# Kernel optimization log

Measured on AMD Instinct MI355X. Metric: run time of the kernel, lower is better.

The kernel has to match this reference:

```python
import jax, jax.numpy as jnp
import numpy as np

N = 50000
E = 800000
HID = 128
EIN = 2 * HID + 1  # h[row] ++ h[col] ++ edge_attr
NC = 3             # n_coords
DIM = 3            # spatial dim
NORM_FACTOR = 100.0
LN_EPS = 1e-5


def layernorm(x, g, b):
    m = jnp.mean(x, axis=-1, keepdims=True)
    v = jnp.mean(jnp.square(x - m), axis=-1, keepdims=True)
    return (x - m) * jax.lax.rsqrt(v + LN_EPS) * g + b


def setup_inputs() -> dict:
    key = jax.random.key(0)
    ks = jax.random.split(key, 12)
    h = jax.random.normal(ks[0], (N, HID), dtype=jnp.float32)
    coord = jax.random.normal(ks[1], (N, NC, DIM), dtype=jnp.float32)
    coord_diff = jax.random.normal(ks[2], (E, NC, DIM), dtype=jnp.float32)
    edge_attr = jax.random.normal(ks[3], (E, 1), dtype=jnp.float32)
    edge_mask = jnp.ones((E, 1), dtype=jnp.float32)
    node_mask = jnp.ones((N, 1, 1), dtype=jnp.float32)
    row = jax.random.randint(ks[4], (E,), 0, N, dtype=jnp.int32)
    col = jax.random.randint(ks[5], (E,), 0, N, dtype=jnp.int32)
    # MLP params (stored [in, out])
    def xavier(k, fi, fo, gain=1.0):
        lim = gain * np.sqrt(6.0 / (fi + fo))
        return jax.random.uniform(k, (fi, fo), dtype=jnp.float32, minval=-lim, maxval=lim)
    W1 = xavier(ks[6], EIN, HID)
    b1 = jnp.zeros((HID,), jnp.float32)
    g1 = jnp.ones((HID,), jnp.float32)
    be1 = jnp.zeros((HID,), jnp.float32)
    W2 = xavier(ks[7], HID, HID)
    b2 = jnp.zeros((HID,), jnp.float32)
    g2 = jnp.ones((HID,), jnp.float32)
    be2 = jnp.zeros((HID,), jnp.float32)
    W3 = xavier(ks[8], HID, NC * NC, gain=0.01)  # final layer, no bias
    return dict(h=h, coord=coord, coord_diff=coord_diff, edge_attr=edge_attr,
                edge_mask=edge_mask, node_mask=node_mask, row=row, col=col,
                W1=W1, b1=b1, g1=g1, be1=be1, W2=W2, b2=b2, g2=g2, be2=be2, W3=W3)


def reference(h, coord, coord_diff, edge_attr, edge_mask, node_mask, row, col,
              W1, b1, g1, be1, W2, b2, g2, be2, W3):
    # gather node feats into edge features: [E, 2*HID + 1]
    x = jnp.concatenate([h[row], h[col], edge_attr], axis=1)
    x = jax.nn.silu(layernorm(x @ W1 + b1, g1, be1))
    x = jax.nn.silu(layernorm(x @ W2 + b2, g2, be2))
    phi = (x @ W3).reshape(-1, NC, NC)               # [E, NC, NC]
    trans = jnp.einsum('ejk,ejl->elk', coord_diff, phi)  # [E, NC, DIM]
    trans = trans * edge_mask[:, None]               # [E,1,1] broadcast
    agg = jax.ops.segment_sum(trans, row, num_segments=coord.shape[0]) / NORM_FACTOR
    return (coord + agg) * node_mask
```

## Files before the change

kernel.cpp:

```cpp
#include <hip/hip_runtime.h>
#include <hip/hip_bf16.h>

#define NN 50000
#define EE 800000

typedef __attribute__((ext_vector_type(8))) short short8;
typedef __attribute__((ext_vector_type(4))) short short4v;
typedef __attribute__((ext_vector_type(4))) float f32x4;

__device__ __forceinline__ float bf2f(ushort u) {
  union { unsigned u; float f; } v; v.u = ((unsigned)u) << 16; return v.f;
}
__device__ __forceinline__ ushort f2bf(float f) {
  union { float f; unsigned u; } v; v.f = f;
  unsigned r = v.u + 0x7FFFu + ((v.u >> 16) & 1u);
  return (ushort)(r >> 16);
}
__device__ __forceinline__ float silu(float v) {
  return v * __builtin_amdgcn_rcpf(1.f + __expf(-v));
}

__global__ void prep_kernel(const float* __restrict__ W1, const float* __restrict__ W2,
                            const float* __restrict__ W3,
                            ushort* __restrict__ W1at, ushort* __restrict__ W1bt,
                            ushort* __restrict__ W2t, ushort* __restrict__ W3t,
                            float* __restrict__ agg) {
  int b = blockIdx.x, tid = threadIdx.x;
  if (b < 200) {
    int i = b * 256 + tid;
    if (i < 16384) {
      int n = i >> 7, k = i & 127;
      W1at[i] = f2bf(W1[k*128 + n]);
    } else if (i < 32768) {
      int j = i - 16384, n = j >> 7, k = j & 127;
      W1bt[j] = f2bf(W1[(k + 128)*128 + n]);
    } else if (i < 49152) {
      int j = i - 32768, n = j >> 7, k = j & 127;
      W2t[j] = f2bf(W2[k*128 + n]);
    } else if (i < 51200) {
      int j = i - 49152, n = j >> 7, k = j & 127;
      W3t[j] = (n < 9) ? f2bf(W3[k*9 + n]) : (ushort)0;
    }
  } else {
    int i = (b - 200) * 256 + tid;
    if (i < NN*9) agg[i] = 0.f;
  }
}

template<bool PQF32>
__global__ __launch_bounds__(256, 4)
void node_kernel(const float* __restrict__ h,
                 const ushort* __restrict__ W1at, const ushort* __restrict__ W1bt,
                 const float* __restrict__ b1,
                 void* __restrict__ Pv, void* __restrict__ Qv) {
  __shared__ __align__(16) ushort smH[64*128];
  const int tid = threadIdx.x;
  const int lane = tid & 63;
  const int w   = tid >> 6;
  const int l15 = lane & 15;
  const int lh  = lane >> 4;
  const int wm  = w >> 1;
  const int wn  = w & 1;
  const int n0  = blockIdx.x * 64;

  {
    int e = tid >> 2, p = tid & 3;
    int nn = n0 + e; if (nn >= NN) nn = NN - 1;
    const float* s = h + (size_t)nn*128 + p*32;
    #pragma unroll
    for (int c = 0; c < 4; ++c) {
      float4 a = *(const float4*)(s + c*8);
      float4 bq = *(const float4*)(s + c*8 + 4);
      short8 v;
      v[0]=f2bf(a.x); v[1]=f2bf(a.y); v[2]=f2bf(a.z); v[3]=f2bf(a.w);
      v[4]=f2bf(bq.x); v[5]=f2bf(bq.y); v[6]=f2bf(bq.z); v[7]=f2bf(bq.w);
      int bo = (e*256 + p*64 + c*16) ^ ((e & 7) << 4);
      *(short8*)((char*)smH + bo) = v;
    }
  }
  __syncthreads();

  const ushort* W = wm ? W1bt : W1at;
  f32x4 acc[4][2] = {};
  #pragma unroll
  for (int k0 = 0; k0 < 4; ++k0) {
    short8 a[4], b[2];
    #pragma unroll
    for (int mf = 0; mf < 4; ++mf)
      a[mf] = *(const short8*)(W + (size_t)(mf*16 + l15)*128 + k0*32 + lh*8);
    #pragma unroll
    for (int nf = 0; nf < 2; ++nf) {
      int e = wn*32 + nf*16 + l15;
      int bo = (e*256 + k0*64 + lh*16) ^ ((e & 7) << 4);
      b[nf] = *(const short8*)((char*)smH + bo);
    }
    #pragma unroll
    for (int mf = 0; mf < 4; ++mf)
      #pragma unroll
      for (int nf = 0; nf < 2; ++nf)
        acc[mf][nf] = __builtin_amdgcn_mfma_f32_16x16x32_bf16(a[mf], b[nf], acc[mf][nf], 0, 0, 0);
  }

  #pragma unroll
  for (int mf = 0; mf < 4; ++mf) {
    float4 bq = *(const float4*)(b1 + mf*16 + lh*4);
    #pragma unroll
    for (int nf = 0; nf < 2; ++nf) {
      int node = n0 + wn*32 + nf*16 + l15;
      if (node < NN) {
        f32x4 r = acc[mf][nf];
        if (wm == 0) { r[0]+=bq.x; r[1]+=bq.y; r[2]+=bq.z; r[3]+=bq.w; }
        if (PQF32) {
          float* dst = (float*)(wm ? Qv : Pv) + (size_t)node*128 + mf*16 + lh*4;
          *(f32x4*)dst = r;
        } else {
          ushort* dst = (ushort*)(wm ? Qv : Pv) + (size_t)node*128 + mf*16 + lh*4;
          short4v o; o[0]=f2bf(r[0]); o[1]=f2bf(r[1]); o[2]=f2bf(r[2]); o[3]=f2bf(r[3]);
          *(short4v*)dst = o;
        }
      }
    }
  }
}

template<bool PQF32>
__global__ __launch_bounds__(256, 6)
void edge_kernel(const void* __restrict__ Pv, const void* __restrict__ Qv,
                 const float* __restrict__ w1last,
                 const float* __restrict__ g1, const float* __restrict__ be1,
                 const ushort* __restrict__ W2t, const ushort* __restrict__ W3t,
                 const float* __restrict__ b2, const float* __restrict__ g2, const float* __restrict__ be2,
                 const float* __restrict__ edge_attr, const float* __restrict__ edge_mask,
                 const float* __restrict__ coord_diff,
                 const int* __restrict__ row, const int* __restrict__ col,
                 float* __restrict__ agg) {
  __shared__ __align__(16) char smem[25344];
  ushort* smX   = (ushort*)smem;
  float*  smPhi = (float*)(smem + 16384);
  float*  smCd  = (float*)(smem + 21504);
  float2* smRed = (float2*)(smem + 23808);
  float*  smEM  = (float*)(smem + 24832);
  int*    smRow = (int*)  (smem + 25088);

  const int tid  = threadIdx.x;
  const int lane = tid & 63;
  const int w    = tid >> 6;
  const int l15  = lane & 15;
  const int lh   = lane >> 4;
  const int wm   = w >> 1;
  const int wn   = w & 1;
  const int e0   = blockIdx.x * 64;
  const int nb   = wm*64 + lh*4;

  {
    int e = tid >> 2, p = tid & 3;
    int re = row[e0 + e], ce = col[e0 + e];
    float ea = edge_attr[e0 + e];
    if (p == 0) { smEM[e] = edge_mask[e0+e]; smRow[e] = re; }

    float v[32]; float s = 0.f, q = 0.f;
    if (PQF32) {
      const float* Pp = (const float*)Pv + (size_t)re*128 + p*32;
      const float* Qp = (const float*)Qv + (size_t)ce*128 + p*32;
      #pragma unroll
      for (int c = 0; c < 8; ++c) {
        float4 a = *(const float4*)(Pp + c*4);
        float4 bq = *(const float4*)(Qp + c*4);
        float4 wq = *(const float4*)(w1last + p*32 + c*4);
        #pragma unroll
        for (int j = 0; j < 4; ++j) {
          float t = ((const float*)&a)[j] + ((const float*)&bq)[j] + ea * ((const float*)&wq)[j];
          v[c*4 + j] = t; s += t; q += t*t;
        }
      }
    } else {
      const ushort* Pp = (const ushort*)Pv + (size_t)re*128 + p*32;
      const ushort* Qp = (const ushort*)Qv + (size_t)ce*128 + p*32;
      #pragma unroll
      for (int c = 0; c < 4; ++c) {
        short8 a = *(const short8*)(Pp + c*8);
        short8 bq = *(const short8*)(Qp + c*8);
        float4 wq0 = *(const float4*)(w1last + p*32 + c*8);
        float4 wq1 = *(const float4*)(w1last + p*32 + c*8 + 4);
        #pragma unroll
        for (int j = 0; j < 8; ++j) {
          float wv = (j < 4) ? ((const float*)&wq0)[j] : ((const float*)&wq1)[j-4];
          float t = bf2f((ushort)a[j]) + bf2f((ushort)bq[j]) + ea * wv;
          v[c*8 + j] = t; s += t; q += t*t;
        }
      }
    }
    s += __shfl_xor(s, 1, 64); s += __shfl_xor(s, 2, 64);
    q += __shfl_xor(q, 1, 64); q += __shfl_xor(q, 2, 64);
    float m  = s * (1.f/128.f);
    float rs = rsqrtf(q * (1.f/128.f) - m*m + 1e-5f);
    #pragma unroll
    for (int c = 0; c < 4; ++c) {
      float4 gq0 = *(const float4*)(g1 + p*32 + c*8);
      float4 gq1 = *(const float4*)(g1 + p*32 + c*8 + 4);
      float4 bq0 = *(const float4*)(be1 + p*32 + c*8);
      float4 bq1 = *(const float4*)(be1 + p*32 + c*8 + 4);
      short8 o;
      #pragma unroll
      for (int j = 0; j < 8; ++j) {
        float gv = (j < 4) ? ((const float*)&gq0)[j] : ((const float*)&gq1)[j-4];
        float bv = (j < 4) ? ((const float*)&bq0)[j] : ((const float*)&bq1)[j-4];
        float val = (v[c*8+j] - m) * rs * gv + bv;
        o[j] = f2bf(silu(val));
      }
      int bo = (e*256 + p*64 + c*16) ^ ((e & 7) << 4);
      *(short8*)((char*)smX + bo) = o;
    }
  }
  if (tid < 144)
    *(float4*)(smCd + tid*4) = *(const float4*)(coord_diff + (size_t)e0*9 + tid*4);
  __syncthreads();

  f32x4 acc2[4][2] = {};
  {
    const ushort* A2 = W2t + (size_t)(wm*64 + l15) * 128 + lh*8;
    #pragma unroll
    for (int k0 = 0; k0 < 4; ++k0) {
      short8 a[4], b[2];
      #pragma unroll
      for (int mf = 0; mf < 4; ++mf) a[mf] = *(const short8*)(A2 + mf*2048 + k0*32);
      #pragma unroll
      for (int nf = 0; nf < 2; ++nf) {
        int e = wn*32 + nf*16 + l15;
        int bo = (e*256 + k0*64 + lh*16) ^ ((e & 7) << 4);
        b[nf] = *(const short8*)((char*)smX + bo);
      }
      #pragma unroll
      for (int mf = 0; mf < 4; ++mf)
        #pragma unroll
        for (int nf = 0; nf < 2; ++nf)
          acc2[mf][nf] = __builtin_amdgcn_mfma_f32_16x16x32_bf16(a[mf], b[nf], acc2[mf][nf], 0, 0, 0);
    }
  }

  float s2[2] = {0.f, 0.f}, q2[2] = {0.f, 0.f};
  #pragma unroll
  for (int mf = 0; mf < 4; ++mf) {
    float4 b2q = *(const float4*)(b2 + nb + mf*16);
    #pragma unroll
    for (int nf = 0; nf < 2; ++nf)
      #pragma unroll
      for (int j = 0; j < 4; ++j) {
        float t = acc2[mf][nf][j] + ((const float*)&b2q)[j];
        acc2[mf][nf][j] = t; s2[nf] += t; q2[nf] += t*t;
      }
  }
  #pragma unroll
  for (int nf = 0; nf < 2; ++nf) {
    s2[nf] += __shfl_xor(s2[nf], 16, 64); s2[nf] += __shfl_xor(s2[nf], 32, 64);
    q2[nf] += __shfl_xor(q2[nf], 16, 64); q2[nf] += __shfl_xor(q2[nf], 32, 64);
  }
  if (lh == 0) {
    #pragma unroll
    for (int nf = 0; nf < 2; ++nf)
      smRed[((wm*2 + wn)*2 + nf)*16 + l15] = make_float2(s2[nf], q2[nf]);
  }
  __syncthreads();

  {
    float m[2], rs[2];
    #pragma unroll
    for (int nf = 0; nf < 2; ++nf) {
      float2 po = smRed[(((wm^1)*2 + wn)*2 + nf)*16 + l15];
      float S = s2[nf] + po.x, Q = q2[nf] + po.y;
      m[nf] = S * (1.f/128.f);
      rs[nf] = rsqrtf(Q * (1.f/128.f) - m[nf]*m[nf] + 1e-5f);
    }
    #pragma unroll
    for (int mf = 0; mf < 4; ++mf) {
      float4 gq  = *(const float4*)(g2 + nb + mf*16);
      float4 beq = *(const float4*)(be2 + nb + mf*16);
      #pragma unroll
      for (int nf = 0; nf < 2; ++nf) {
        int e = wn*32 + nf*16 + l15;
        short4v o;
        #pragma unroll
        for (int j = 0; j < 4; ++j) {
          float val = (acc2[mf][nf][j] - m[nf]) * rs[nf] * ((const float*)&gq)[j] + ((const float*)&beq)[j];
          o[j] = f2bf(silu(val));
        }
        int bo = (e*256 + (nb + mf*16)*2) ^ ((e & 7) << 4);
        *(short4v*)((char*)smX + bo) = o;
      }
    }
  }
  __syncthreads();

  {
    f32x4 acc3 = {};
    const ushort* A3 = W3t + (size_t)l15 * 128 + lh*8;
    int e = w*16 + l15;
    #pragma unroll
    for (int k0 = 0; k0 < 4; ++k0) {
      short8 a = *(const short8*)(A3 + k0*32);
      int bo = (e*256 + k0*64 + lh*16) ^ ((e & 7) << 4);
      short8 b = *(const short8*)((char*)smX + bo);
      acc3 = __builtin_amdgcn_mfma_f32_16x16x32_bf16(a, b, acc3, 0, 0, 0);
    }
    *(float4*)(smPhi + e*20 + lh*4) = *(float4*)&acc3;
  }
  __syncthreads();

  {
    int e = tid >> 2, qd = tid & 3;
    int re = smRow[e];
    float em = smEM[e];
    const float* cd = smCd + e*9;
    const float* ph = smPhi + e*20;
    for (int idx = qd; idx < 9; idx += 4) {
      int l2 = idx / 3, k = idx - l2*3;
      float t = cd[k]*ph[l2] + cd[3+k]*ph[3+l2] + cd[6+k]*ph[6+l2];
      unsafeAtomicAdd(&agg[(size_t)re*9 + idx], t * em);
    }
  }
}

__global__ void finalize_kernel(const float* __restrict__ coord, const float* __restrict__ node_mask,
                                const float* __restrict__ agg, float* __restrict__ out) {
  int i = blockIdx.x * 256 + threadIdx.x;
  if (i < NN*9) {
    int n = i / 9;
    out[i] = (coord[i] + agg[i] * 0.01f) * node_mask[n];
  }
}

extern "C" void kernel_launch(void* const* d_in, const int* in_sizes, int n_in,
                              void* d_out, int out_size, void* d_ws, size_t ws_size,
                              hipStream_t stream) {
  const float* h          = (const float*)d_in[0];
  const float* coord      = (const float*)d_in[1];
  const float* coord_diff = (const float*)d_in[2];
  const float* edge_attr  = (const float*)d_in[3];
  const float* edge_mask  = (const float*)d_in[4];
  const float* node_mask  = (const float*)d_in[5];
  const int*   rowi       = (const int*)d_in[6];
  const int*   coli       = (const int*)d_in[7];
  const float* W1  = (const float*)d_in[8];
  const float* b1  = (const float*)d_in[9];
  const float* g1  = (const float*)d_in[10];
  const float* be1 = (const float*)d_in[11];
  const float* W2  = (const float*)d_in[12];
  const float* b2  = (const float*)d_in[13];
  const float* g2  = (const float*)d_in[14];
  const float* be2 = (const float*)d_in[15];
  const float* W3  = (const float*)d_in[16];
  const float* w1last = W1 + 256*128;

  char* ws = (char*)d_ws;
  const size_t needF32 = 53102400;
  const int nodeBlocks = (NN + 63) / 64;
  const int aggBlocks  = (NN*9 + 255) / 256;

  if (ws_size >= needF32) {
    float*  P    = (float*)ws;
    float*  Q    = (float*)(ws + 25600000);
    float*  agg  = (float*)(ws + 51200000);
    ushort* W1at = (ushort*)(ws + 53000000);
    ushort* W1bt = (ushort*)(ws + 53032768);
    ushort* W2t  = (ushort*)(ws + 53065536);
    ushort* W3t  = (ushort*)(ws + 53098304);
    prep_kernel<<<200 + aggBlocks, 256, 0, stream>>>(W1, W2, W3, W1at, W1bt, W2t, W3t, agg);
    node_kernel<true><<<nodeBlocks, 256, 0, stream>>>(h, W1at, W1bt, b1, P, Q);
    edge_kernel<true><<<EE/64, 256, 0, stream>>>(P, Q, w1last, g1, be1, W2t, W3t,
        b2, g2, be2, edge_attr, edge_mask, coord_diff, rowi, coli, agg);
    finalize_kernel<<<aggBlocks, 256, 0, stream>>>(coord, node_mask, agg, (float*)d_out);
  } else {
    ushort* P    = (ushort*)ws;
    ushort* Q    = (ushort*)(ws + 12800000);
    float*  agg  = (float*)(ws + 25600000);
    ushort* W1at = (ushort*)(ws + 27400000);
    ushort* W1bt = (ushort*)(ws + 27432768);
    ushort* W2t  = (ushort*)(ws + 27465536);
    ushort* W3t  = (ushort*)(ws + 27498304);
    prep_kernel<<<200 + aggBlocks, 256, 0, stream>>>(W1, W2, W3, W1at, W1bt, W2t, W3t, agg);
    node_kernel<false><<<nodeBlocks, 256, 0, stream>>>(h, W1at, W1bt, b1, P, Q);
    edge_kernel<false><<<EE/64, 256, 0, stream>>>(P, Q, w1last, g1, be1, W2t, W3t,
        b2, g2, be2, edge_attr, edge_mask, coord_diff, rowi, coli, agg);
    finalize_kernel<<<aggBlocks, 256, 0, stream>>>(coord, node_mask, agg, (float*)d_out);
  }
}
```

Baseline: 536.3 us.

## Make edge kernel wave-local with bf16 P/Q and no block barriers

```diff
diff --git a/kernel.cpp b/kernel.cpp
--- a/kernel.cpp
+++ b/kernel.cpp
@@ -47,12 +47,11 @@
   }
 }
 
-template<bool PQF32>
 __global__ __launch_bounds__(256, 4)
 void node_kernel(const float* __restrict__ h,
                  const ushort* __restrict__ W1at, const ushort* __restrict__ W1bt,
                  const float* __restrict__ b1,
-                 void* __restrict__ Pv, void* __restrict__ Qv) {
+                 ushort* __restrict__ P, ushort* __restrict__ Q) {
   __shared__ __align__(16) ushort smH[64*128];
   const int tid = threadIdx.x;
   const int lane = tid & 63;
@@ -110,22 +109,16 @@
       if (node < NN) {
         f32x4 r = acc[mf][nf];
         if (wm == 0) { r[0]+=bq.x; r[1]+=bq.y; r[2]+=bq.z; r[3]+=bq.w; }
-        if (PQF32) {
-          float* dst = (float*)(wm ? Qv : Pv) + (size_t)node*128 + mf*16 + lh*4;
-          *(f32x4*)dst = r;
-        } else {
-          ushort* dst = (ushort*)(wm ? Qv : Pv) + (size_t)node*128 + mf*16 + lh*4;
-          short4v o; o[0]=f2bf(r[0]); o[1]=f2bf(r[1]); o[2]=f2bf(r[2]); o[3]=f2bf(r[3]);
-          *(short4v*)dst = o;
-        }
+        ushort* dst = (wm ? Q : P) + (size_t)node*128 + mf*16 + lh*4;
+        short4v o; o[0]=f2bf(r[0]); o[1]=f2bf(r[1]); o[2]=f2bf(r[2]); o[3]=f2bf(r[3]);
+        *(short4v*)dst = o;
       }
     }
   }
 }
 
-template<bool PQF32>
-__global__ __launch_bounds__(256, 6)
-void edge_kernel(const void* __restrict__ Pv, const void* __restrict__ Qv,
+__global__ __launch_bounds__(256, 4)
+void edge_kernel(const ushort* __restrict__ P, const ushort* __restrict__ Q,
                  const float* __restrict__ w1last,
                  const float* __restrict__ g1, const float* __restrict__ be1,
                  const ushort* __restrict__ W2t, const ushort* __restrict__ W3t,
@@ -134,60 +127,46 @@
                  const float* __restrict__ coord_diff,
                  const int* __restrict__ row, const int* __restrict__ col,
                  float* __restrict__ agg) {
-  __shared__ __align__(16) char smem[25344];
+  __shared__ __align__(16) char smem[23808];
   ushort* smX   = (ushort*)smem;
   float*  smPhi = (float*)(smem + 16384);
   float*  smCd  = (float*)(smem + 21504);
-  float2* smRed = (float2*)(smem + 23808);
-  float*  smEM  = (float*)(smem + 24832);
-  int*    smRow = (int*)  (smem + 25088);
 
   const int tid  = threadIdx.x;
   const int lane = tid & 63;
   const int w    = tid >> 6;
   const int l15  = lane & 15;
   const int lh   = lane >> 4;
-  const int wm   = w >> 1;
-  const int wn   = w & 1;
   const int e0   = blockIdx.x * 64;
-  const int nb   = wm*64 + lh*4;
+  const int we   = w * 16;
 
   {
     int e = tid >> 2, p = tid & 3;
-    int re = row[e0 + e], ce = col[e0 + e];
-    float ea = edge_attr[e0 + e];
-    if (p == 0) { smEM[e] = edge_mask[e0+e]; smRow[e] = re; }
+    int ge = e0 + e;
+    int re = row[ge], ce = col[ge];
+    float ea = edge_attr[ge];
+    const ushort* Pp = P + (size_t)re*128 + p*32;
+    const ushort* Qp = Q + (size_t)ce*128 + p*32;
+    short8 pa[4], qa[4];
+    #pragma unroll
+    for (int c = 0; c < 4; ++c) pa[c] = *(const short8*)(Pp + c*8);
+    #pragma unroll
+    for (int c = 0; c < 4; ++c) qa[c] = *(const short8*)(Qp + c*8);
+
+    if (lane < 36)
+      *(float4*)(smCd + we*9 + lane*4) =
+          *(const float4*)(coord_diff + (size_t)(e0 + we)*9 + lane*4);
 
     float v[32]; float s = 0.f, q = 0.f;
-    if (PQF32) {
-      const float* Pp = (const float*)Pv + (size_t)re*128 + p*32;
-      const float* Qp = (const float*)Qv + (size_t)ce*128 + p*32;
+    #pragma unroll
+    for (int c = 0; c < 4; ++c) {
+      float4 wq0 = *(const float4*)(w1last + p*32 + c*8);
+      float4 wq1 = *(const float4*)(w1last + p*32 + c*8 + 4);
       #pragma unroll
-      for (int c = 0; c < 8; ++c) {
-        float4 a = *(const float4*)(Pp + c*4);
-        float4 bq = *(const float4*)(Qp + c*4);
-        float4 wq = *(const float4*)(w1last + p*32 + c*4);
-        #pragma unroll
-        for (int j = 0; j < 4; ++j) {
-          float t = ((const float*)&a)[j] + ((const float*)&bq)[j] + ea * ((const float*)&wq)[j];
-          v[c*4 + j] = t; s += t; q += t*t;
-        }
-      }
-    } else {
-      const ushort* Pp = (const ushort*)Pv + (size_t)re*128 + p*32;
-      const ushort* Qp = (const ushort*)Qv + (size_t)ce*128 + p*32;
-      #pragma unroll
-      for (int c = 0; c < 4; ++c) {
-        short8 a = *(const short8*)(Pp + c*8);
-        short8 bq = *(const short8*)(Qp + c*8);
-        float4 wq0 = *(const float4*)(w1last + p*32 + c*8);
-        float4 wq1 = *(const float4*)(w1last + p*32 + c*8 + 4);
-        #pragma unroll
-        for (int j = 0; j < 8; ++j) {
-          float wv = (j < 4) ? ((const float*)&wq0)[j] : ((const float*)&wq1)[j-4];
-          float t = bf2f((ushort)a[j]) + bf2f((ushort)bq[j]) + ea * wv;
-          v[c*8 + j] = t; s += t; q += t*t;
-        }
+      for (int j = 0; j < 8; ++j) {
+        float wv = (j < 4) ? ((const float*)&wq0)[j] : ((const float*)&wq1)[j-4];
+        float t = bf2f((ushort)pa[c][j]) + bf2f((ushort)qa[c][j]) + ea * wv;
+        v[c*8 + j] = t; s += t; q += t*t;
       }
     }
     s += __shfl_xor(s, 1, 64); s += __shfl_xor(s, 2, 64);
@@ -212,110 +191,81 @@
       *(short8*)((char*)smX + bo) = o;
     }
   }
-  if (tid < 144)
-    *(float4*)(smCd + tid*4) = *(const float4*)(coord_diff + (size_t)e0*9 + tid*4);
-  __syncthreads();
-
-  f32x4 acc2[4][2] = {};
+  asm volatile("s_waitcnt lgkmcnt(0)" ::: "memory");
+  __builtin_amdgcn_sched_barrier(0);
+
+  const int e2 = we + l15;
+
+  f32x4 acc2[8] = {};
+  #pragma unroll
+  for (int k0 = 0; k0 < 4; ++k0) {
+    int bo = (e2*256 + k0*64 + lh*16) ^ ((e2 & 7) << 4);
+    short8 bfrag = *(const short8*)((char*)smX + bo);
+    #pragma unroll
+    for (int mf = 0; mf < 8; ++mf) {
+      short8 a = *(const short8*)(W2t + (size_t)(mf*16 + l15)*128 + k0*32 + lh*8);
+      acc2[mf] = __builtin_amdgcn_mfma_f32_16x16x32_bf16(a, bfrag, acc2[mf], 0, 0, 0);
+    }
+  }
+
+  float s2 = 0.f, q2 = 0.f;
+  #pragma unroll
+  for (int mf = 0; mf < 8; ++mf) {
+    float4 bq = *(const float4*)(b2 + mf*16 + lh*4);
+    #pragma unroll
+    for (int j = 0; j < 4; ++j) {
+      float t = acc2[mf][j] + ((const float*)&bq)[j];
+      acc2[mf][j] = t; s2 += t; q2 += t*t;
+    }
+  }
+  s2 += __shfl_xor(s2, 16, 64); s2 += __shfl_xor(s2, 32, 64);
+  q2 += __shfl_xor(q2, 16, 64); q2 += __shfl_xor(q2, 32, 64);
   {
-    const ushort* A2 = W2t + (size_t)(wm*64 + l15) * 128 + lh*8;
-    #pragma unroll
-    for (int k0 = 0; k0 < 4; ++k0) {
-      short8 a[4], b[2];
-      #pragma unroll
-      for (int mf = 0; mf < 4; ++mf) a[mf] = *(const short8*)(A2 + mf*2048 + k0*32);
-      #pragma unroll
-      for (int nf = 0; nf < 2; ++nf) {
-        int e = wn*32 + nf*16 + l15;
-        int bo = (e*256 + k0*64 + lh*16) ^ ((e & 7) << 4);
-        b[nf] = *(const short8*)((char*)smX + bo);
-      }
-      #pragma unroll
-      for (int mf = 0; mf < 4; ++mf)
-        #pragma unroll
-        for (int nf = 0; nf < 2; ++nf)
-          acc2[mf][nf] = __builtin_amdgcn_mfma_f32_16x16x32_bf16(a[mf], b[nf], acc2[mf][nf], 0, 0, 0);
-    }
-  }
-
-  float s2[2] = {0.f, 0.f}, q2[2] = {0.f, 0.f};
-  #pragma unroll
-  for (int mf = 0; mf < 4; ++mf) {
-    float4 b2q = *(const float4*)(b2 + nb + mf*16);
-    #pragma unroll
-    for (int nf = 0; nf < 2; ++nf)
+    float m  = s2 * (1.f/128.f);
+    float rs = rsqrtf(q2 * (1.f/128.f) - m*m + 1e-5f);
+    #pragma unroll
+    for (int mf = 0; mf < 8; ++mf) {
+      float4 gq  = *(const float4*)(g2 + mf*16 + lh*4);
+      float4 beq = *(const float4*)(be2 + mf*16 + lh*4);
+      short4v o;
       #pragma unroll
       for (int j = 0; j < 4; ++j) {
-        float t = acc2[mf][nf][j] + ((const float*)&b2q)[j];
-        acc2[mf][nf][j] = t; s2[nf] += t; q2[nf] += t*t;
+        float val = (acc2[mf][j] - m) * rs * ((const float*)&gq)[j] + ((const float*)&beq)[j];
+        o[j] = f2bf(silu(val));
       }
-  }
-  #pragma unroll
-  for (int nf = 0; nf < 2; ++nf) {
-    s2[nf] += __shfl_xor(s2[nf], 16, 64); s2[nf] += __shfl_xor(s2[nf], 32, 64);
-    q2[nf] += __shfl_xor(q2[nf], 16, 64); q2[nf] += __shfl_xor(q2[nf], 32, 64);
-  }
-  if (lh == 0) {
-    #pragma unroll
-    for (int nf = 0; nf < 2; ++nf)
-      smRed[((wm*2 + wn)*2 + nf)*16 + l15] = make_float2(s2[nf], q2[nf]);
-  }
-  __syncthreads();
-
-  {
-    float m[2], rs[2];
-    #pragma unroll
-    for (int nf = 0; nf < 2; ++nf) {
-      float2 po = smRed[(((wm^1)*2 + wn)*2 + nf)*16 + l15];
-      float S = s2[nf] + po.x, Q = q2[nf] + po.y;
-      m[nf] = S * (1.f/128.f);
-      rs[nf] = rsqrtf(Q * (1.f/128.f) - m[nf]*m[nf] + 1e-5f);
-    }
-    #pragma unroll
-    for (int mf = 0; mf < 4; ++mf) {
-      float4 gq  = *(const float4*)(g2 + nb + mf*16);
-      float4 beq = *(const float4*)(be2 + nb + mf*16);
-      #pragma unroll
-      for (int nf = 0; nf < 2; ++nf) {
-        int e = wn*32 + nf*16 + l15;
-        short4v o;
-        #pragma unroll
-        for (int j = 0; j < 4; ++j) {
-          float val = (acc2[mf][nf][j] - m[nf]) * rs[nf] * ((const float*)&gq)[j] + ((const float*)&beq)[j];
-          o[j] = f2bf(silu(val));
-        }
-        int bo = (e*256 + (nb + mf*16)*2) ^ ((e & 7) << 4);
-        *(short4v*)((char*)smX + bo) = o;
-      }
-    }
-  }
-  __syncthreads();
+      int bo = (e2*256 + (mf*16 + lh*4)*2) ^ ((e2 & 7) << 4);
+      *(short4v*)((char*)smX + bo) = o;
+    }
+  }
+  asm volatile("s_waitcnt lgkmcnt(0)" ::: "memory");
+  __builtin_amdgcn_sched_barrier(0);
 
   {
     f32x4 acc3 = {};
     const ushort* A3 = W3t + (size_t)l15 * 128 + lh*8;
-    int e = w*16 + l15;
     #pragma unroll
     for (int k0 = 0; k0 < 4; ++k0) {
       short8 a = *(const short8*)(A3 + k0*32);
-      int bo = (e*256 + k0*64 + lh*16) ^ ((e & 7) << 4);
+      int bo = (e2*256 + k0*64 + lh*16) ^ ((e2 & 7) << 4);
       short8 b = *(const short8*)((char*)smX + bo);
       acc3 = __builtin_amdgcn_mfma_f32_16x16x32_bf16(a, b, acc3, 0, 0, 0);
     }
-    *(float4*)(smPhi + e*20 + lh*4) = *(float4*)&acc3;
-  }
-  __syncthreads();
-
-  {
-    int e = tid >> 2, qd = tid & 3;
-    int re = smRow[e];
-    float em = smEM[e];
-    const float* cd = smCd + e*9;
-    const float* ph = smPhi + e*20;
-    for (int idx = qd; idx < 9; idx += 4) {
-      int l2 = idx / 3, k = idx - l2*3;
-      float t = cd[k]*ph[l2] + cd[3+k]*ph[3+l2] + cd[6+k]*ph[6+l2];
-      unsafeAtomicAdd(&agg[(size_t)re*9 + idx], t * em);
+    *(float4*)(smPhi + e2*20 + lh*4) = *(float4*)&acc3;
+  }
+  asm volatile("s_waitcnt lgkmcnt(0)" ::: "memory");
+  __builtin_amdgcn_sched_barrier(0);
+
+  if (lh < 3) {
+    int ge = e0 + e2;
+    int re = row[ge];
+    float em = edge_mask[ge];
+    const float* cd = smCd + e2*9;
+    const float* ph = smPhi + e2*20;
+    int l = lh;
+    #pragma unroll
+    for (int k = 0; k < 3; ++k) {
+      float t = cd[k]*ph[l] + cd[3+k]*ph[3+l] + cd[6+k]*ph[6+l];
+      unsafeAtomicAdd(&agg[(size_t)re*9 + l*3 + k], t * em);
     }
   }
 }
@@ -352,35 +302,20 @@
   const float* w1last = W1 + 256*128;
 
   char* ws = (char*)d_ws;
-  const size_t needF32 = 53102400;
+  ushort* P    = (ushort*)ws;
+  ushort* Q    = (ushort*)(ws + 12800000);
+  float*  agg  = (float*)(ws + 25600000);
+  ushort* W1at = (ushort*)(ws + 27400192);
+  ushort* W1bt = (ushort*)(ws + 27432960);
+  ushort* W2t  = (ushort*)(ws + 27465728);
+  ushort* W3t  = (ushort*)(ws + 27498496);
+
   const int nodeBlocks = (NN + 63) / 64;
   const int aggBlocks  = (NN*9 + 255) / 256;
 
-  if (ws_size >= needF32) {
-    float*  P    = (float*)ws;
-    float*  Q    = (float*)(ws + 25600000);
-    float*  agg  = (float*)(ws + 51200000);
-    ushort* W1at = (ushort*)(ws + 53000000);
-    ushort* W1bt = (ushort*)(ws + 53032768);
-    ushort* W2t  = (ushort*)(ws + 53065536);
-    ushort* W3t  = (ushort*)(ws + 53098304);
-    prep_kernel<<<200 + aggBlocks, 256, 0, stream>>>(W1, W2, W3, W1at, W1bt, W2t, W3t, agg);
-    node_kernel<true><<<nodeBlocks, 256, 0, stream>>>(h, W1at, W1bt, b1, P, Q);
-    edge_kernel<true><<<EE/64, 256, 0, stream>>>(P, Q, w1last, g1, be1, W2t, W3t,
-        b2, g2, be2, edge_attr, edge_mask, coord_diff, rowi, coli, agg);
-    finalize_kernel<<<aggBlocks, 256, 0, stream>>>(coord, node_mask, agg, (float*)d_out);
-  } else {
-    ushort* P    = (ushort*)ws;
-    ushort* Q    = (ushort*)(ws + 12800000);
-    float*  agg  = (float*)(ws + 25600000);
-    ushort* W1at = (ushort*)(ws + 27400000);
-    ushort* W1bt = (ushort*)(ws + 27432768);
-    ushort* W2t  = (ushort*)(ws + 27465536);
-    ushort* W3t  = (ushort*)(ws + 27498304);
-    prep_kernel<<<200 + aggBlocks, 256, 0, stream>>>(W1, W2, W3, W1at, W1bt, W2t, W3t, agg);
-    node_kernel<false><<<nodeBlocks, 256, 0, stream>>>(h, W1at, W1bt, b1, P, Q);
-    edge_kernel<false><<<EE/64, 256, 0, stream>>>(P, Q, w1last, g1, be1, W2t, W3t,
-        b2, g2, be2, edge_attr, edge_mask, coord_diff, rowi, coli, agg);
-    finalize_kernel<<<aggBlocks, 256, 0, stream>>>(coord, node_mask, agg, (float*)d_out);
-  }
-}
+  prep_kernel<<<200 + aggBlocks, 256, 0, stream>>>(W1, W2, W3, W1at, W1bt, W2t, W3t, agg);
+  node_kernel<<<nodeBlocks, 256, 0, stream>>>(h, W1at, W1bt, b1, P, Q);
+  edge_kernel<<<EE/64, 256, 0, stream>>>(P, Q, w1last, g1, be1, W2t, W3t,
+      b2, g2, be2, edge_attr, edge_mask, coord_diff, rowi, coli, agg);
+  finalize_kernel<<<aggBlocks, 256, 0, stream>>>(coord, node_mask, agg, (float*)d_out);
+}
```

Result: slower. 554.6 us (+3.4%).
